# Performance work log

Measured on AMD Instinct MI355X. Metric: run time of the kernel, lower is better.

## Reference

```python
import jax, jax.numpy as jnp
import numpy as np


def _avgpool2(x):
    # 2x2 average pool, stride 2 (NCHW)
    n, c, h, w = x.shape
    return x.reshape(n, c, h // 2, 2, w // 2, 2).mean(axis=(3, 5))


def setup_inputs() -> dict:
    key = jax.random.key(0)
    k1, k2, k3, k4 = jax.random.split(key, 4)
    N, H, W = 32, 512, 512
    N2 = H // 4
    eps = 1e-4  # keep probabilities strictly inside (0,1) for BCE
    logits = jax.random.uniform(k1, (N, 1, H, W), jnp.float32, eps, 1.0 - eps)
    labels = jax.random.uniform(k2, (N, 1, H, W), jnp.float32, eps, 1.0 - eps)
    v_attention = jax.random.uniform(k3, (N, 1, N2, N2), jnp.float32)
    h_attention = jax.random.uniform(k4, (N, 1, N2, N2), jnp.float32)
    return {"logits": logits, "labels": labels,
            "v_attention": v_attention, "h_attention": h_attention}


def reference(logits, labels, v_attention, h_attention):
    N = labels.shape[0]
    smooth = 1.0

    # --- BCE over all elements ---
    p = logits.reshape(-1)
    y = labels.reshape(-1)
    bceloss = -jnp.mean(y * jnp.log(p) + (1.0 - y) * jnp.log(1.0 - p))

    # --- Dice on thresholded logits ---
    masks = (logits > 0.4).astype(logits.dtype)
    input_flat = masks.reshape(N, -1)
    target_flat = labels.reshape(N, -1)
    intersection = (input_flat * target_flat).sum(axis=1)
    dice = 2.0 * (intersection + smooth) / (input_flat.sum(axis=1) + target_flat.sum(axis=1) + smooth)
    diceloss = 1.0 - dice.sum() / N

    # --- Per-sample 3-way Pearson-style correlation ---
    N1 = v_attention.shape[0]
    attent_labels = _avgpool2(_avgpool2(labels))          # [N,1,H/4,W/4]
    v = v_attention.reshape(N1, -1)                        # [N1, N2*N2]
    h = h_attention.reshape(N1, -1)
    l = attent_labels.reshape(N1, -1)
    vc = v - v.mean(axis=1, keepdims=True)
    hc = h - h.mean(axis=1, keepdims=True)
    lc = l - l.mean(axis=1, keepdims=True)
    num = (vc * hc * lc).sum(axis=1)
    den = jnp.sqrt((vc * vc).sum(axis=1) * (hc * hc).sum(axis=1) * (lc * lc).sum(axis=1))
    cor_loss = -(num / den).sum() / N1

    return 0.2 * bceloss + 0.3 * diceloss + 0.5 * cor_loss
```

## Files before the change

kernel.cpp:

```cpp
#include <hip/hip_runtime.h>
#include <math.h>

#define NSAMP 32
#define HW 512
#define PW 128
#define NPOOL (PW * PW)
#define BPS 8
#define NBLOCKS (NSAMP * BPS)
#define PPT 8
#define NACC 14


__device__ __forceinline__ float wave_sum_dpp(float x) {
#define DPP_ADD(ctrl)                                                         \
    x += __int_as_float(__builtin_amdgcn_update_dpp(                          \
        0, __float_as_int(x), (ctrl), 0xf, 0xf, true));
    DPP_ADD(0x111)
    DPP_ADD(0x112)
    DPP_ADD(0x114)
    DPP_ADD(0x118)
    DPP_ADD(0x142)
    DPP_ADD(0x143)
#undef DPP_ADD
    return x;
}

__global__ __launch_bounds__(256) void covloss_main(
    const float* __restrict__ logits, const float* __restrict__ labels,
    const float* __restrict__ v_att,  const float* __restrict__ h_att,
    float* __restrict__ part)
{
    const int bid   = blockIdx.x;
    const int n     = bid >> 3;
    const int local = bid & 7;

    const float* lg = logits + (size_t)n * HW * HW;
    const float* lb = labels + (size_t)n * HW * HW;
    const float* va = v_att + (size_t)n * NPOOL;
    const float* ha = h_att + (size_t)n * NPOOL;

    float bce = 0.f, inter = 0.f, ysum = 0.f;
    unsigned long long cnt_u = 0;
    float S_v = 0.f, S_h = 0.f, S_l = 0.f;
    float S_vv = 0.f, S_hh = 0.f, S_ll = 0.f;
    float S_vh = 0.f, S_vl = 0.f, S_hl = 0.f, S_vhl = 0.f;

#pragma unroll
    for (int p = 0; p < PPT; ++p) {
        const int pidx = local * (PPT * 256) + p * 256 + threadIdx.x;
        const int pr = pidx >> 7;
        const int pc = pidx & 127;
        const float4* lg4 = (const float4*)(lg + (size_t)(4 * pr) * HW) + pc;
        const float4* lb4 = (const float4*)(lb + (size_t)(4 * pr) * HW) + pc;
        const float v = va[pidx];
        const float h = ha[pidx];

        float lsum = 0.f;
#pragma unroll
        for (int i = 0; i < 4; ++i) {
            const float4 p4 = lg4[i * (HW / 4)];
            const float4 y4 = lb4[i * (HW / 4)];
            const float pv[4] = {p4.x, p4.y, p4.z, p4.w};
            const float yv[4] = {y4.x, y4.y, y4.z, y4.w};
#pragma unroll
            for (int j = 0; j < 4; ++j) {
                const float pp = pv[j], y = yv[j];
                bce = fmaf(y, __log2f(pp), bce);
                bce = fmaf(1.f - y, __log2f(1.f - pp), bce);
                const bool m = pp > 0.4f;
                cnt_u += __popcll(__ballot(m));
                inter += m ? y : 0.f;
                lsum  += y;
            }
        }
        ysum += lsum;
        const float l = lsum * 0.0625f;
        S_v += v;          S_h += h;          S_l += l;
        S_vv = fmaf(v, v, S_vv);  S_hh = fmaf(h, h, S_hh);  S_ll = fmaf(l, l, S_ll);
        const float vh = v * h;
        S_vh += vh;        S_vl = fmaf(v, l, S_vl);  S_hl = fmaf(h, l, S_hl);
        S_vhl = fmaf(vh, l, S_vhl);
    }

    float vals[13] = { bce, inter, ysum,
                       S_v, S_h, S_l, S_vv, S_hh, S_ll,
                       S_vh, S_vl, S_hl, S_vhl };

#pragma unroll
    for (int k = 0; k < 13; ++k) vals[k] = wave_sum_dpp(vals[k]);

    __shared__ float sh[4][NACC];
    const int lane = threadIdx.x & 63, wv = threadIdx.x >> 6;
    if (lane == 63) {
        sh[wv][0] = vals[0];
        sh[wv][1] = (float)cnt_u;
        sh[wv][2] = vals[1];
        sh[wv][3] = vals[2];
#pragma unroll
        for (int k = 3; k < 13; ++k) sh[wv][k + 1] = vals[k];
    }
    __syncthreads();
    if (threadIdx.x < NACC) {
        part[(size_t)threadIdx.x * NBLOCKS + bid] =
            sh[0][threadIdx.x] + sh[1][threadIdx.x] + sh[2][threadIdx.x] + sh[3][threadIdx.x];
    }
}

__global__ __launch_bounds__(256) void covloss_finalize(
    const float* __restrict__ part, float* __restrict__ out)
{
    const int t = threadIdx.x;
    __shared__ double acc[NSAMP][NACC];

    for (int pair = t; pair < NSAMP * NACC; pair += 256) {
        const int s = pair / NACC, k = pair % NACC;
        const float4* p = (const float4*)(part + (size_t)k * NBLOCKS + s * BPS);
        double a = 0.0;
#pragma unroll
        for (int i = 0; i < 2; ++i) {
            const float4 q = p[i];
            a += (double)q.x + (double)q.y + (double)q.z + (double)q.w;
        }
        acc[s][k] = a;
    }
    __syncthreads();

    __shared__ double sb[NSAMP], sd[NSAMP], sc[NSAMP];
    if (t < NSAMP) {
        const double* a = acc[t];
        const double nn = (double)NPOOL;
        const double cvv = a[7] - a[4] * a[4] / nn;
        const double chh = a[8] - a[5] * a[5] / nn;
        const double cll = a[9] - a[6] * a[6] / nn;
        const double num = a[13]
            - (a[4] * a[12] + a[5] * a[11] + a[6] * a[10]) / nn
            + 2.0 * a[4] * a[5] * a[6] / (nn * nn);
        sc[t] = num / sqrt(cvv * chh * cll);
        sd[t] = 2.0 * (a[2] + 1.0) / (a[1] + a[3] + 1.0);
        sb[t] = a[0];
    }
    __syncthreads();
    if (t == 0) {
        double bces = 0.0, ds = 0.0, cs = 0.0;
#pragma unroll
        for (int i = 0; i < NSAMP; ++i) { bces += sb[i]; ds += sd[i]; cs += sc[i]; }
        const double bceloss = -(bces * M_LN2) / ((double)NSAMP * HW * HW);
        out[0] = (float)(0.2 * bceloss + 0.3 * (1.0 - ds / NSAMP) + 0.5 * (-cs / NSAMP));
    }
}

extern "C" void kernel_launch(void* const* d_in, const int* in_sizes, int n_in,
                              void* d_out, int out_size, void* d_ws, size_t ws_size,
                              hipStream_t stream) {
    const float* logits = (const float*)d_in[0];
    const float* labels = (const float*)d_in[1];
    const float* v_att  = (const float*)d_in[2];
    const float* h_att  = (const float*)d_in[3];
    float* out  = (float*)d_out;
    float* part = (float*)d_ws;

    covloss_main<<<NBLOCKS, 256, 0, stream>>>(logits, labels, v_att, h_att, part);
    covloss_finalize<<<1, 256, 0, stream>>>(part, out);
}
```

Measured before the change: 22.92 us.

## Fuse finalize into main kernel via atomic fixed-point accumulation and last-block reduction

Replaces the separate finalize launch with a last-block-done pattern: each block atomically adds fixed-point int64 partials per sample, increments a global counter, and the final block computes the loss. The grid is doubled with half the pooled pixels per thread, and all global loads in an iteration are issued before compute to raise memory-level parallelism. This adds a memset of the workspace and atomic traffic, and relies on fixed-point scaling to stay within range and precision.

After: 28.33 us. 1.24x slower.

```diff
diff --git a/kernel.cpp b/kernel.cpp
--- a/kernel.cpp
+++ b/kernel.cpp
@@ -5,10 +5,12 @@
 #define HW 512
 #define PW 128
 #define NPOOL (PW * PW)
-#define BPS 8
+#define BPS 16
 #define NBLOCKS (NSAMP * BPS)
-#define PPT 8
+#define PPT 4
 #define NACC 14
+#define FP_SCALE 1073741824.0
+#define FP_INV   (1.0 / 1073741824.0)
 
 
 __device__ __forceinline__ float wave_sum_dpp(float x) {
@@ -25,14 +27,17 @@
     return x;
 }
 
-__global__ __launch_bounds__(256) void covloss_main(
+__global__ __launch_bounds__(256) void covloss_fused(
     const float* __restrict__ logits, const float* __restrict__ labels,
     const float* __restrict__ v_att,  const float* __restrict__ h_att,
-    float* __restrict__ part)
+    float* __restrict__ out, unsigned long long* __restrict__ ws)
 {
+    unsigned long long* counter = ws;
+    unsigned long long* cells   = ws + 8;
+
     const int bid   = blockIdx.x;
-    const int n     = bid >> 3;
-    const int local = bid & 7;
+    const int n     = bid >> 4;
+    const int local = bid & 15;
 
     const float* lg = logits + (size_t)n * HW * HW;
     const float* lb = labels + (size_t)n * HW * HW;
@@ -52,16 +57,20 @@
         const int pc = pidx & 127;
         const float4* lg4 = (const float4*)(lg + (size_t)(4 * pr) * HW) + pc;
         const float4* lb4 = (const float4*)(lb + (size_t)(4 * pr) * HW) + pc;
+
+        float4 P[4], Y[4];
+#pragma unroll
+        for (int i = 0; i < 4; ++i) P[i] = lg4[i * (HW / 4)];
+#pragma unroll
+        for (int i = 0; i < 4; ++i) Y[i] = lb4[i * (HW / 4)];
         const float v = va[pidx];
         const float h = ha[pidx];
 
         float lsum = 0.f;
 #pragma unroll
         for (int i = 0; i < 4; ++i) {
-            const float4 p4 = lg4[i * (HW / 4)];
-            const float4 y4 = lb4[i * (HW / 4)];
-            const float pv[4] = {p4.x, p4.y, p4.z, p4.w};
-            const float yv[4] = {y4.x, y4.y, y4.z, y4.w};
+            const float pv[4] = {P[i].x, P[i].y, P[i].z, P[i].w};
+            const float yv[4] = {Y[i].x, Y[i].y, Y[i].z, Y[i].w};
 #pragma unroll
             for (int j = 0; j < 4; ++j) {
                 const float pp = pv[j], y = yv[j];
@@ -85,7 +94,6 @@
     float vals[13] = { bce, inter, ysum,
                        S_v, S_h, S_l, S_vv, S_hh, S_ll,
                        S_vh, S_vl, S_hl, S_vhl };
-
 #pragma unroll
     for (int k = 0; k < 13; ++k) vals[k] = wave_sum_dpp(vals[k]);
 
@@ -100,28 +108,29 @@
         for (int k = 3; k < 13; ++k) sh[wv][k + 1] = vals[k];
     }
     __syncthreads();
+
     if (threadIdx.x < NACC) {
-        part[(size_t)threadIdx.x * NBLOCKS + bid] =
-            sh[0][threadIdx.x] + sh[1][threadIdx.x] + sh[2][threadIdx.x] + sh[3][threadIdx.x];
+        const double d = (double)(sh[0][threadIdx.x] + sh[1][threadIdx.x] +
+                                  sh[2][threadIdx.x] + sh[3][threadIdx.x]);
+        const long long q = __double2ll_rn(d * FP_SCALE);
+        atomicAdd(&cells[n * NACC + threadIdx.x], (unsigned long long)q);
     }
-}
 
-__global__ __launch_bounds__(256) void covloss_finalize(
-    const float* __restrict__ part, float* __restrict__ out)
-{
+    __shared__ int lastflag;
+    if (threadIdx.x == 0) {
+        __builtin_amdgcn_s_waitcnt(0);
+        const unsigned long long old = atomicAdd(counter, 1ULL);
+        lastflag = (old == NBLOCKS - 1);
+    }
+    __syncthreads();
+    if (!lastflag) return;
+
     const int t = threadIdx.x;
     __shared__ double acc[NSAMP][NACC];
-
-    for (int pair = t; pair < NSAMP * NACC; pair += 256) {
-        const int s = pair / NACC, k = pair % NACC;
-        const float4* p = (const float4*)(part + (size_t)k * NBLOCKS + s * BPS);
-        double a = 0.0;
-#pragma unroll
-        for (int i = 0; i < 2; ++i) {
-            const float4 q = p[i];
-            a += (double)q.x + (double)q.y + (double)q.z + (double)q.w;
-        }
-        acc[s][k] = a;
+    for (int c = t; c < NSAMP * NACC; c += 256) {
+        const unsigned long long u =
+            __hip_atomic_load(&cells[c], __ATOMIC_RELAXED, __HIP_MEMORY_SCOPE_AGENT);
+        ((double*)acc)[c] = (double)(long long)u * FP_INV;
     }
     __syncthreads();
 
@@ -156,9 +165,9 @@
     const float* labels = (const float*)d_in[1];
     const float* v_att  = (const float*)d_in[2];
     const float* h_att  = (const float*)d_in[3];
-    float* out  = (float*)d_out;
-    float* part = (float*)d_ws;
+    float* out = (float*)d_out;
+    unsigned long long* ws = (unsigned long long*)d_ws;
 
-    covloss_main<<<NBLOCKS, 256, 0, stream>>>(logits, labels, v_att, h_att, part);
-    covloss_finalize<<<1, 256, 0, stream>>>(part, out);
+    hipMemsetAsync(d_ws, 0, 8 * 8 + (size_t)NSAMP * NACC * 8, stream);
+    covloss_fused<<<NBLOCKS, 256, 0, stream>>>(logits, labels, v_att, h_att, out, ws);
 }
```

## Double the grid and software-pipeline loads with three register buffers

Applied to the files above, without the earlier changes.

Doubles the block count to 512 (16 per sample), so each thread handles 4 pooled pixels instead of 8. The inner loop becomes an explicit three-buffer register pipeline: three groups of loads are issued before any compute, and the fourth group's loads are issued after the first compute. The aim is more memory-level parallelism and better latency hiding on a bandwidth-bound reduction. The cost is higher register pressure, with launch bounds asking for 2 blocks per CU, and twice as many partials for the finalize kernel to sum.

Result: faster. 20.68 us (-9.8%).

```diff
diff --git a/kernel.cpp b/kernel.cpp
--- a/kernel.cpp
+++ b/kernel.cpp
@@ -5,9 +5,9 @@
 #define HW 512
 #define PW 128
 #define NPOOL (PW * PW)
-#define BPS 8
+#define BPS 16
 #define NBLOCKS (NSAMP * BPS)
-#define PPT 8
+#define PPT 4
 #define NACC 14
 
 
@@ -25,14 +25,15 @@
     return x;
 }
 
-__global__ __launch_bounds__(256) void covloss_main(
+__global__ __launch_bounds__(256, 2) void covloss_main(
     const float* __restrict__ logits, const float* __restrict__ labels,
     const float* __restrict__ v_att,  const float* __restrict__ h_att,
     float* __restrict__ part)
 {
     const int bid   = blockIdx.x;
-    const int n     = bid >> 3;
-    const int local = bid & 7;
+    const int n     = bid >> 4;
+    const int local = bid & 15;
+    const int pbase = local * (PPT * 256);
 
     const float* lg = logits + (size_t)n * HW * HW;
     const float* lb = labels + (size_t)n * HW * HW;
@@ -45,47 +46,62 @@
     float S_vv = 0.f, S_hh = 0.f, S_ll = 0.f;
     float S_vh = 0.f, S_vl = 0.f, S_hl = 0.f, S_vhl = 0.f;
 
-#pragma unroll
-    for (int p = 0; p < PPT; ++p) {
-        const int pidx = local * (PPT * 256) + p * 256 + threadIdx.x;
-        const int pr = pidx >> 7;
-        const int pc = pidx & 127;
-        const float4* lg4 = (const float4*)(lg + (size_t)(4 * pr) * HW) + pc;
-        const float4* lb4 = (const float4*)(lb + (size_t)(4 * pr) * HW) + pc;
-        const float v = va[pidx];
-        const float h = ha[pidx];
+    float4 PA[4], YA[4]; float vA, hA;
+    float4 PB[4], YB[4]; float vB, hB;
+    float4 PC[4], YC[4]; float vC, hC;
 
-        float lsum = 0.f;
-#pragma unroll
-        for (int i = 0; i < 4; ++i) {
-            const float4 p4 = lg4[i * (HW / 4)];
-            const float4 y4 = lb4[i * (HW / 4)];
-            const float pv[4] = {p4.x, p4.y, p4.z, p4.w};
-            const float yv[4] = {y4.x, y4.y, y4.z, y4.w};
-#pragma unroll
-            for (int j = 0; j < 4; ++j) {
-                const float pp = pv[j], y = yv[j];
-                bce = fmaf(y, __log2f(pp), bce);
-                bce = fmaf(1.f - y, __log2f(1.f - pp), bce);
-                const bool m = pp > 0.4f;
-                cnt_u += __popcll(__ballot(m));
-                inter += m ? y : 0.f;
-                lsum  += y;
-            }
-        }
-        ysum += lsum;
-        const float l = lsum * 0.0625f;
-        S_v += v;          S_h += h;          S_l += l;
-        S_vv = fmaf(v, v, S_vv);  S_hh = fmaf(h, h, S_hh);  S_ll = fmaf(l, l, S_ll);
-        const float vh = v * h;
-        S_vh += vh;        S_vl = fmaf(v, l, S_vl);  S_hl = fmaf(h, l, S_hl);
-        S_vhl = fmaf(vh, l, S_vhl);
-    }
+#define LOADBUF(S, p) {                                                       \
+    const int pidx = pbase + (p) * 256 + (int)threadIdx.x;                    \
+    const int pr = pidx >> 7, pc = pidx & 127;                                \
+    const float4* lg4 = (const float4*)(lg + (size_t)(4 * pr) * HW) + pc;     \
+    const float4* lb4 = (const float4*)(lb + (size_t)(4 * pr) * HW) + pc;     \
+    P##S[0] = lg4[0]; P##S[1] = lg4[HW / 4];                                  \
+    P##S[2] = lg4[2 * (HW / 4)]; P##S[3] = lg4[3 * (HW / 4)];                 \
+    Y##S[0] = lb4[0]; Y##S[1] = lb4[HW / 4];                                  \
+    Y##S[2] = lb4[2 * (HW / 4)]; Y##S[3] = lb4[3 * (HW / 4)];                 \
+    v##S = va[pidx]; h##S = ha[pidx]; }
+
+#define COMPUTE(S) {                                                          \
+    float lsum = 0.f;                                                         \
+    _Pragma("unroll")                                                         \
+    for (int i = 0; i < 4; ++i) {                                             \
+        const float pv[4] = {P##S[i].x, P##S[i].y, P##S[i].z, P##S[i].w};     \
+        const float yv[4] = {Y##S[i].x, Y##S[i].y, Y##S[i].z, Y##S[i].w};     \
+        _Pragma("unroll")                                                     \
+        for (int j = 0; j < 4; ++j) {                                         \
+            const float pp = pv[j], y = yv[j];                                \
+            bce = fmaf(y, __log2f(pp), bce);                                  \
+            bce = fmaf(1.f - y, __log2f(1.f - pp), bce);                      \
+            const bool m = pp > 0.4f;                                         \
+            cnt_u += __popcll(__ballot(m));                                   \
+            inter += m ? y : 0.f;                                             \
+            lsum  += y;                                                       \
+        }                                                                     \
+    }                                                                         \
+    ysum += lsum;                                                             \
+    const float l = lsum * 0.0625f;                                           \
+    const float v = v##S, h = h##S;                                           \
+    S_v += v; S_h += h; S_l += l;                                             \
+    S_vv = fmaf(v, v, S_vv); S_hh = fmaf(h, h, S_hh); S_ll = fmaf(l, l, S_ll);\
+    const float vh = v * h;                                                   \
+    S_vh += vh; S_vl = fmaf(v, l, S_vl); S_hl = fmaf(h, l, S_hl);             \
+    S_vhl = fmaf(vh, l, S_vhl); }
+
+    LOADBUF(A, 0)
+    LOADBUF(B, 1)
+    LOADBUF(C, 2)
+    COMPUTE(A)
+    LOADBUF(A, 3)
+    COMPUTE(B)
+    COMPUTE(C)
+    COMPUTE(A)
+
+#undef LOADBUF
+#undef COMPUTE
 
     float vals[13] = { bce, inter, ysum,
                        S_v, S_h, S_l, S_vv, S_hh, S_ll,
                        S_vh, S_vl, S_hl, S_vhl };
-
 #pragma unroll
     for (int k = 0; k < 13; ++k) vals[k] = wave_sum_dpp(vals[k]);
 
@@ -117,7 +133,7 @@
         const float4* p = (const float4*)(part + (size_t)k * NBLOCKS + s * BPS);
         double a = 0.0;
 #pragma unroll
-        for (int i = 0; i < 2; ++i) {
+        for (int i = 0; i < 4; ++i) {
             const float4 q = p[i];
             a += (double)q.x + (double)q.y + (double)q.z + (double)q.w;
         }
```
